# Performance work log

Measured on AMD Instinct MI355X. Metric: run time of the kernel, lower is better.

## Reference

```python
import jax, jax.numpy as jnp
import numpy as np

B, S, DM, H, D = 2, 2048, 1024, 16, 64

def setup_inputs() -> dict:
    key = jax.random.key(0)
    ks = jax.random.split(key, 9)
    def g(k, shape, scale=0.02):
        return jax.random.normal(k, shape, dtype=jnp.float32) * scale
    return {
        "x":  jax.random.normal(ks[0], (B, S, DM), dtype=jnp.float32),
        "Wq": g(ks[1], (DM, H * D)), "bq": g(ks[2], (H * D,)),
        "Wk": g(ks[3], (DM, H * D)), "bk": g(ks[4], (H * D,)),
        "Wv": g(ks[5], (DM, H * D)), "bv": g(ks[6], (H * D,)),
        "Wo": g(ks[7], (H * D, DM)), "bo": g(ks[8], (DM,)),
    }

def reference(x, Wq, bq, Wk, bk, Wv, bv, Wo, bo):
    b, s, _ = x.shape
    # projections -> (B, H, S, D)
    q = (x @ Wq + bq).reshape(b, s, H, D).transpose(0, 2, 1, 3)
    k = (x @ Wk + bk).reshape(b, s, H, D).transpose(0, 2, 1, 3)
    v = (x @ Wv + bv).reshape(b, s, H, D).transpose(0, 2, 1, 3)
    # naive attention: full (B,H,S,S) scores, causal mask, softmax
    scores = jnp.einsum("bhqd,bhkd->bhqk", q, k) / jnp.sqrt(jnp.float32(D))
    causal = jnp.tril(jnp.ones((s, s), dtype=bool))
    scores = jnp.where(causal[None, None], scores, jnp.float32(-jnp.inf))
    weights = jax.nn.softmax(scores, axis=-1)
    out = jnp.einsum("bhqk,bhkd->bhqd", weights, v)  # (B,H,S,D)
    out = out.transpose(0, 2, 1, 3).reshape(b, s, H * D)
    return out @ Wo + bo  # dropout_p = 0 -> identity
```

## Files before the change

### kernel.cpp

```cpp
#include <hip/hip_runtime.h>
#include <hip/hip_bf16.h>

typedef __hip_bfloat16 bf16;
typedef __attribute__((ext_vector_type(8))) short bf16x8;
typedef __attribute__((ext_vector_type(4))) float f32x4;
typedef __attribute__((ext_vector_type(4))) unsigned int u32x4;

#define MFMA_BF16(a, b, c) __builtin_amdgcn_mfma_f32_16x16x32_bf16((a), (b), (c), 0, 0, 0)

static constexpr int B_  = 2;
static constexpr int S_  = 2048;
static constexpr int DM_ = 1024;
static constexpr int H_  = 16;
static constexpr int D_  = 64;
static constexpr int M_  = B_ * S_;

__device__ __forceinline__ void load16(const void* g, void* l) {
  __builtin_amdgcn_global_load_lds(
      (const __attribute__((address_space(1))) void*)g,
      (__attribute__((address_space(3))) void*)l, 16, 0, 0);
}

__device__ __forceinline__ unsigned int pack_bf16(float lo, float hi) {
  const unsigned int ul = __builtin_bit_cast(unsigned short, __float2bfloat16(lo));
  const unsigned int uh = __builtin_bit_cast(unsigned short, __float2bfloat16(hi));
  return (uh << 16) | ul;
}

__global__ void prep_kernel(const float* __restrict__ w0,
                            const float* __restrict__ w1,
                            const float* __restrict__ w2,
                            const float* __restrict__ w3,
                            const float* __restrict__ x,
                            bf16* __restrict__ o0, bf16* __restrict__ o1,
                            bf16* __restrict__ o2, bf16* __restrict__ o3,
                            bf16* __restrict__ xb) {
  if (blockIdx.z == 4) {
    const int blk = blockIdx.y * 32 + blockIdx.x;
#pragma unroll
    for (int rep = 0; rep < 4; ++rep) {
      const int i = blk * 1024 + rep * 256 + threadIdx.x;
      float4 v = ((const float4*)x)[i];
      ushort4 u;
      u.x = __builtin_bit_cast(unsigned short, __float2bfloat16(v.x));
      u.y = __builtin_bit_cast(unsigned short, __float2bfloat16(v.y));
      u.z = __builtin_bit_cast(unsigned short, __float2bfloat16(v.z));
      u.w = __builtin_bit_cast(unsigned short, __float2bfloat16(v.w));
      ((ushort4*)xb)[i] = u;
    }
    return;
  }
  __shared__ float t[32][33];
  const float* in = blockIdx.z == 0 ? w0 : blockIdx.z == 1 ? w1 : blockIdx.z == 2 ? w2 : w3;
  bf16* out = blockIdx.z == 0 ? o0 : blockIdx.z == 1 ? o1 : blockIdx.z == 2 ? o2 : o3;
  int tx = threadIdx.x & 31;
  int ty = threadIdx.x >> 5;
  int r0 = blockIdx.y * 32;
  int c0 = blockIdx.x * 32;
#pragma unroll
  for (int yy = 0; yy < 32; yy += 8)
    t[ty + yy][tx] = in[(size_t)(r0 + ty + yy) * DM_ + c0 + tx];
  __syncthreads();
#pragma unroll
  for (int yy = 0; yy < 32; yy += 8)
    out[(size_t)(c0 + ty + yy) * DM_ + r0 + tx] = __float2bfloat16(t[tx][ty + yy]);
}

__global__ __launch_bounds__(256) void gemm_qkv_kernel(
    const bf16* __restrict__ A, const bf16* __restrict__ Bt,
    const float* __restrict__ bias, const float* __restrict__ bias2,
    const float* __restrict__ bias3, bf16* __restrict__ out, int K) {
  __shared__ bf16 As[2][128 * 32];
  __shared__ bf16 Bs[2][128 * 32];
  const int tid = threadIdx.x;
  const int wid = tid >> 6, lane = tid & 63;
  const int g = lane >> 4, c = lane & 15;
  const int wr = wid >> 1, wc = wid & 1;
  const int bm = blockIdx.x, bn = blockIdx.y;

  f32x4 acc[4][4] = {};

  const char* Ag = (const char*)(A + (size_t)bm * 128 * K);
  const char* Bg = (const char*)(Bt + (size_t)bn * 128 * K);
  const int f0 = tid * 16, f1 = f0 + 4096;
  const int r0 = f0 >> 6, cb0 = f0 & 63;
  const int r1 = f1 >> 6;
  const size_t rowbytes = (size_t)K * 2;

  auto stage = [&](int kt, int bufi) {
    const size_t koff = (size_t)kt * 64;
    load16(Ag + (size_t)r0 * rowbytes + koff + cb0, (char*)As[bufi] + f0);
    load16(Ag + (size_t)r1 * rowbytes + koff + cb0, (char*)As[bufi] + f1);
    load16(Bg + (size_t)r0 * rowbytes + koff + cb0, (char*)Bs[bufi] + f0);
    load16(Bg + (size_t)r1 * rowbytes + koff + cb0, (char*)Bs[bufi] + f1);
  };

  const int NT = K / 32;
  stage(0, 0);
  int cur = 0;
#pragma unroll 1
  for (int kt = 0; kt < NT; ++kt) {
    if (kt + 1 < NT) {
      stage(kt + 1, cur ^ 1);
      asm volatile("s_waitcnt vmcnt(4)" ::: "memory");
    } else {
      asm volatile("s_waitcnt vmcnt(0)" ::: "memory");
    }
    __builtin_amdgcn_s_barrier();

    bf16x8 af[4], bfr[4];
#pragma unroll
    for (int mi = 0; mi < 4; ++mi)
      af[mi] = *(const bf16x8*)&As[cur][(wr * 64 + mi * 16 + c) * 32 + g * 8];
#pragma unroll
    for (int ni = 0; ni < 4; ++ni)
      bfr[ni] = *(const bf16x8*)&Bs[cur][(wc * 64 + ni * 16 + c) * 32 + g * 8];
    __builtin_amdgcn_s_setprio(1);
#pragma unroll
    for (int mi = 0; mi < 4; ++mi)
#pragma unroll
      for (int ni = 0; ni < 4; ++ni)
        acc[mi][ni] = MFMA_BF16(af[mi], bfr[ni], acc[mi][ni]);
    __builtin_amdgcn_s_setprio(0);

    if (kt + 1 < NT) __builtin_amdgcn_s_barrier();
    cur ^= 1;
  }

#pragma unroll
  for (int ni = 0; ni < 4; ++ni) {
    const int n_g = bn * 128 + wc * 64 + ni * 16 + c;
    const int proj = n_g >> 10, ncol = n_g & 1023;
    const float bv = proj == 0 ? bias[ncol] : proj == 1 ? bias2[ncol] : bias3[ncol];
    const int h = ncol >> 6, d = ncol & (D_ - 1);
#pragma unroll
    for (int mi = 0; mi < 4; ++mi) {
#pragma unroll
      for (int r = 0; r < 4; ++r) {
        const int m_g = bm * 128 + wr * 64 + mi * 16 + g * 4 + r;
        const float val = acc[mi][ni][r] + bv;
        const int b = m_g >> 11, s = m_g & (S_ - 1);
        size_t idx = (size_t)proj * 4194304;
        if (proj < 2)
          idx += (((size_t)(b * H_ + h)) * S_ + s) * D_ + d;
        else
          idx += (((size_t)(b * H_ + h)) * D_ + d) * S_ + s;
        out[idx] = __float2bfloat16(val);
      }
    }
  }
}

__global__ __launch_bounds__(256) void gemm_out_kernel(
    const bf16* __restrict__ A, const bf16* __restrict__ Bt,
    const float* __restrict__ bias, float* __restrict__ out, int K) {
  __shared__ bf16 As[2][128 * 32];
  __shared__ bf16 Bs[2][64 * 32];
  const int tid = threadIdx.x;
  const int wid = tid >> 6, lane = tid & 63;
  const int g = lane >> 4, c = lane & 15;
  const int wr = wid >> 1, wc = wid & 1;
  const int bm = blockIdx.x, bn = blockIdx.y;

  f32x4 acc[4][2] = {};

  const char* Ag = (const char*)(A + (size_t)bm * 128 * K);
  const char* Bg = (const char*)(Bt + (size_t)bn * 64 * K);
  const int s0 = tid, s1 = tid + 256;
  const int ra0 = s0 >> 2, ca0 = (s0 & 3) * 16;
  const int ra1 = s1 >> 2, ca1 = (s1 & 3) * 16;
  const int rb = tid >> 2, cb2 = (tid & 3) * 16;
  const size_t rowbytes = (size_t)K * 2;

  auto stage = [&](int kt, int bufi) {
    const size_t koff = (size_t)kt * 64;
    load16(Ag + (size_t)ra0 * rowbytes + koff + ca0, (char*)As[bufi] + s0 * 16);
    load16(Ag + (size_t)ra1 * rowbytes + koff + ca1, (char*)As[bufi] + s1 * 16);
    load16(Bg + (size_t)rb * rowbytes + koff + cb2, (char*)Bs[bufi] + tid * 16);
  };

  const int NT = K / 32;
  stage(0, 0);
  int cur = 0;
#pragma unroll 1
  for (int kt = 0; kt < NT; ++kt) {
    if (kt + 1 < NT) {
      stage(kt + 1, cur ^ 1);
      asm volatile("s_waitcnt vmcnt(3)" ::: "memory");
    } else {
      asm volatile("s_waitcnt vmcnt(0)" ::: "memory");
    }
    __builtin_amdgcn_s_barrier();

    bf16x8 af[4], bfr[2];
#pragma unroll
    for (int mi = 0; mi < 4; ++mi)
      af[mi] = *(const bf16x8*)&As[cur][(wr * 64 + mi * 16 + c) * 32 + g * 8];
#pragma unroll
    for (int ni = 0; ni < 2; ++ni)
      bfr[ni] = *(const bf16x8*)&Bs[cur][(wc * 32 + ni * 16 + c) * 32 + g * 8];
    __builtin_amdgcn_s_setprio(1);
#pragma unroll
    for (int mi = 0; mi < 4; ++mi)
#pragma unroll
      for (int ni = 0; ni < 2; ++ni)
        acc[mi][ni] = MFMA_BF16(af[mi], bfr[ni], acc[mi][ni]);
    __builtin_amdgcn_s_setprio(0);

    if (kt + 1 < NT) __builtin_amdgcn_s_barrier();
    cur ^= 1;
  }

#pragma unroll
  for (int ni = 0; ni < 2; ++ni) {
    const int n_g = bn * 64 + wc * 32 + ni * 16 + c;
    const float bv = bias[n_g];
#pragma unroll
    for (int mi = 0; mi < 4; ++mi) {
#pragma unroll
      for (int r = 0; r < 4; ++r) {
        const int m_g = bm * 128 + wr * 64 + mi * 16 + g * 4 + r;
        out[(size_t)m_g * DM_ + n_g] = acc[mi][ni][r] + bv;
      }
    }
  }
}

__global__ __launch_bounds__(256, 4) void flash_attn_kernel(
    const bf16* __restrict__ Q, const bf16* __restrict__ Kg,
    const bf16* __restrict__ Vt, bf16* __restrict__ Aout) {
  __shared__ bf16 Ks[2][64 * 64];
  __shared__ bf16 Vs[2][64 * 64];
  const int tid = threadIdx.x;
  const int w = tid >> 6, lane = tid & 63;
  const int g = lane >> 4, c = lane & 15;

  const int bid = blockIdx.x;
  const int xcd = bid & 7, loc = bid >> 3;
  const int bh = xcd * 4 + (loc & 3);
  const int u = loc >> 2;
  const int slot = u >> 3, q = u & 7;
  const int j = slot == 0 ? 31 - q : slot == 1 ? 16 + q
              : slot == 2 ? 15 - q : q;
  const int t = j * 4 + w;
  const int b = bh >> 4, h = bh & (H_ - 1);

  const float ALPHA2 = 0.125f * 1.44269504f;
  const float THR2 = 11.5f;
  const float NEG_INF = -__builtin_inff();

  const char* Kbase = (const char*)(Kg + (size_t)bh * S_ * D_);
  const char* Vbase = (const char*)(Vt + (size_t)bh * D_ * S_);
  const int s0 = tid, s1 = tid + 256;
  const int sr0 = s0 >> 3, sq0 = ((s0 & 7) ^ (sr0 & 7)) << 4;
  const int sr1 = s1 >> 3, sq1 = ((s1 & 7) ^ (sr1 & 7)) << 4;

  const bf16* Qp = Q + ((size_t)bh * S_ + t * 16 + c) * D_;
  bf16x8 qf[2];
  qf[0] = *(const bf16x8*)&Qp[g * 8];
  qf[1] = *(const bf16x8*)&Qp[32 + g * 8];

  bf16x8 onesf;
#pragma unroll
  for (int jj = 0; jj < 8; ++jj) onesf[jj] = (short)0x3f80;

  f32x4 o[4] = {};
  f32x4 lacc = {};
  float m = -1000.0f;

  const int rowlim = w * 16 + c;
  const int src0 = ((g & 1) * 2) * 16 + c;
  const int src1 = src0 + 16;
  const bool ghi = (g >= 2);
  const int cs = c & 7;
  int roff[2][4];
#pragma unroll
  for (int kk = 0; kk < 2; ++kk)
#pragma unroll
    for (int n = 0; n < 4; ++n)
      roff[kk][n] = n * 2048 + c * 128 + (((kk * 4 + g) ^ cs) << 4);

  {
    load16(Kbase + sr0 * 128 + sq0, (char*)Ks[0] + s0 * 16);
    load16(Kbase + sr1 * 128 + sq1, (char*)Ks[0] + s1 * 16);
    load16(Vbase + sr0 * 4096 + sq0, (char*)Vs[0] + s0 * 16);
    load16(Vbase + sr1 * 4096 + sq1, (char*)Vs[0] + s1 * 16);
  }
  __syncthreads();

  int cur = 0;
#pragma unroll 1
  for (int kv = 0; kv <= j; ++kv) {
    if (kv < j) {
      const char* Krow = Kbase + (size_t)(kv + 1) * 8192;
      const char* Vcol = Vbase + (size_t)(kv + 1) * 128;
      const int nb = cur ^ 1;
      load16(Krow + sr0 * 128 + sq0, (char*)Ks[nb] + s0 * 16);
      load16(Krow + sr1 * 128 + sq1, (char*)Ks[nb] + s1 * 16);
      load16(Vcol + sr0 * 4096 + sq0, (char*)Vs[nb] + s0 * 16);
      load16(Vcol + sr1 * 4096 + sq1, (char*)Vs[nb] + s1 * 16);
    }

    const char* Kt = (const char*)Ks[cur];
    const char* Vtile = (const char*)Vs[cur];
    bf16x8 kf[2][4];
#pragma unroll
    for (int kk = 0; kk < 2; ++kk)
#pragma unroll
      for (int n = 0; n < 4; ++n)
        kf[kk][n] = *(const bf16x8*)(Kt + roff[kk][n]);

    f32x4 st[4] = {};
    __builtin_amdgcn_s_setprio(1);
#pragma unroll
    for (int n = 0; n < 4; ++n) {
      st[n] = MFMA_BF16(kf[0][n], qf[0], st[n]);
      st[n] = MFMA_BF16(kf[1][n], qf[1], st[n]);
    }
    __builtin_amdgcn_s_setprio(0);

    bf16x8 vf[2][4];
#pragma unroll
    for (int kk = 0; kk < 2; ++kk)
#pragma unroll
      for (int n = 0; n < 4; ++n)
        vf[kk][n] = *(const bf16x8*)(Vtile + roff[kk][n]);

    float aa[4][4];
#pragma unroll
    for (int n = 0; n < 4; ++n)
#pragma unroll
      for (int r = 0; r < 4; ++r)
        aa[n][r] = fmaf(st[n][r], ALPHA2, -m);
    if (kv == j) {
#pragma unroll
      for (int n = 0; n < 4; ++n)
#pragma unroll
        for (int r = 0; r < 4; ++r)
          if (n * 16 + g * 4 + r > rowlim) aa[n][r] = NEG_INF;
    }

    float lm;
    {
      float t0 = fmaxf(fmaxf(aa[0][0], aa[0][1]), fmaxf(aa[0][2], aa[0][3]));
      float t1 = fmaxf(fmaxf(aa[1][0], aa[1][1]), fmaxf(aa[1][2], aa[1][3]));
      float t2 = fmaxf(fmaxf(aa[2][0], aa[2][1]), fmaxf(aa[2][2], aa[2][3]));
      float t3 = fmaxf(fmaxf(aa[3][0], aa[3][1]), fmaxf(aa[3][2], aa[3][3]));
      lm = fmaxf(fmaxf(t0, t1), fmaxf(t2, t3));
    }

    if (__any(lm > THR2)) {
      float dm = fmaxf(lm, __shfl_xor(lm, 16, 64));
      dm = fmaxf(dm, __shfl_xor(dm, 32, 64));
      const float sh = fmaxf(dm, 0.0f);
      const float sc = __builtin_amdgcn_exp2f(-sh);
      m += sh;
#pragma unroll
      for (int r = 0; r < 4; ++r) lacc[r] *= sc;
#pragma unroll
      for (int n = 0; n < 4; ++n)
#pragma unroll
        for (int r = 0; r < 4; ++r) o[n][r] *= sc;
#pragma unroll
      for (int n = 0; n < 4; ++n)
#pragma unroll
        for (int r = 0; r < 4; ++r) aa[n][r] -= sh;
    }

    float p[4][4];
#pragma unroll
    for (int n = 0; n < 4; ++n)
#pragma unroll
      for (int r = 0; r < 4; ++r) p[n][r] = __builtin_amdgcn_exp2f(aa[n][r]);

    unsigned int dw[4][2];
#pragma unroll
    for (int n = 0; n < 4; ++n) {
      dw[n][0] = pack_bf16(p[n][0], p[n][1]);
      dw[n][1] = pack_bf16(p[n][2], p[n][3]);
    }

#pragma unroll
    for (int kk = 0; kk < 2; ++kk) {
      unsigned int bb[4];
      {
        unsigned int lo = __shfl(dw[kk * 2][0], src0, 64);
        unsigned int hi = __shfl(dw[kk * 2 + 1][0], src0, 64);
        bb[0] = ghi ? hi : lo;
      }
      {
        unsigned int lo = __shfl(dw[kk * 2][1], src0, 64);
        unsigned int hi = __shfl(dw[kk * 2 + 1][1], src0, 64);
        bb[1] = ghi ? hi : lo;
      }
      {
        unsigned int lo = __shfl(dw[kk * 2][0], src1, 64);
        unsigned int hi = __shfl(dw[kk * 2 + 1][0], src1, 64);
        bb[2] = ghi ? hi : lo;
      }
      {
        unsigned int lo = __shfl(dw[kk * 2][1], src1, 64);
        unsigned int hi = __shfl(dw[kk * 2 + 1][1], src1, 64);
        bb[3] = ghi ? hi : lo;
      }
      u32x4 bbv = {bb[0], bb[1], bb[2], bb[3]};
      bf16x8 pb = __builtin_bit_cast(bf16x8, bbv);
      __builtin_amdgcn_s_setprio(1);
#pragma unroll
      for (int n = 0; n < 4; ++n) o[n] = MFMA_BF16(vf[kk][n], pb, o[n]);
      lacc = MFMA_BF16(onesf, pb, lacc);
      __builtin_amdgcn_s_setprio(0);
    }

    __syncthreads();
    cur ^= 1;
  }

  const float inv = 1.0f / lacc[0];

  bf16* Arow = Aout + ((size_t)b * S_ + t * 16 + c) * (H_ * D_) + h * D_;
#pragma unroll
  for (int n = 0; n < 4; ++n) {
    ushort4 u2;
    u2.x = __builtin_bit_cast(unsigned short, __float2bfloat16(o[n][0] * inv));
    u2.y = __builtin_bit_cast(unsigned short, __float2bfloat16(o[n][1] * inv));
    u2.z = __builtin_bit_cast(unsigned short, __float2bfloat16(o[n][2] * inv));
    u2.w = __builtin_bit_cast(unsigned short, __float2bfloat16(o[n][3] * inv));
    *(ushort4*)&Arow[n * 16 + g * 4] = u2;
  }
}


extern "C" void kernel_launch(void* const* d_in, const int* in_sizes, int n_in,
                              void* d_out, int out_size, void* d_ws, size_t ws_size,
                              hipStream_t stream) {
  (void)in_sizes; (void)n_in; (void)out_size; (void)ws_size;
  const float* x  = (const float*)d_in[0];
  const float* Wq = (const float*)d_in[1];
  const float* bq = (const float*)d_in[2];
  const float* Wk = (const float*)d_in[3];
  const float* bk = (const float*)d_in[4];
  const float* Wv = (const float*)d_in[5];
  const float* bv = (const float*)d_in[6];
  const float* Wo = (const float*)d_in[7];
  const float* bo = (const float*)d_in[8];
  float* out = (float*)d_out;

  char* ws = (char*)d_ws;
  bf16* xb  = (bf16*)(ws);
  bf16* Wqt = (bf16*)(ws + (8u << 20));
  bf16* Wkt = (bf16*)(ws + (10u << 20));
  bf16* Wvt = (bf16*)(ws + (12u << 20));
  bf16* Wot = (bf16*)(ws + (14u << 20));
  bf16* Qb  = (bf16*)(ws + (16u << 20));
  bf16* Kb  = (bf16*)(ws + (24u << 20));
  bf16* Vtb = (bf16*)(ws + (32u << 20));
  bf16* Ab  = xb;

  prep_kernel<<<dim3(32, 32, 5), 256, 0, stream>>>(
      Wq, Wk, Wv, Wo, x, Wqt, Wkt, Wvt, Wot, xb);

  gemm_qkv_kernel<<<dim3(32, 24), 256, 0, stream>>>(
      xb, Wqt, bq, bk, bv, Qb, DM_);

  flash_attn_kernel<<<dim3(1024), 256, 0, stream>>>(Qb, Kb, Vtb, Ab);

  gemm_out_kernel<<<dim3(32, 16), 256, 0, stream>>>(Ab, Wot, bo, out, DM_);
}
```

Measured before the change: 113.2 us.

## Process two 16-row query tiles per wave to double K/V reuse

Each wave now owns two consecutive 16-row query tiles, so a block covers 128 query rows and each K/V tile loaded into LDS serves twice as many queries. The grid is halved from 1024 to 512 blocks and the diagonal masking is reworked for the wider block, with the longest blocks scheduled first. The aim is to cut LDS fill and global K/V traffic per unit of work. In exchange it doubles the accumulator and score registers, which may lower occupancy under launch_bounds(256,4), and fewer blocks with uneven causal lengths may hurt load balance.

```diff
diff --git a/kernel.cpp b/kernel.cpp
--- a/kernel.cpp
+++ b/kernel.cpp
@@ -238,11 +238,10 @@
   const int bid = blockIdx.x;
   const int xcd = bid & 7, loc = bid >> 3;
   const int bh = xcd * 4 + (loc & 3);
-  const int u = loc >> 2;
-  const int slot = u >> 3, q = u & 7;
-  const int j = slot == 0 ? 31 - q : slot == 1 ? 16 + q
-              : slot == 2 ? 15 - q : q;
-  const int t = j * 4 + w;
+  const int v = 15 - (loc >> 2);
+  const int base = v * 8 + w * 2;
+  const int dtile = base >> 2;
+  const int jtop = 2 * v + 1;
   const int b = bh >> 4, h = bh & (H_ - 1);
 
   const float ALPHA2 = 0.125f * 1.44269504f;
@@ -255,20 +254,23 @@
   const int sr0 = s0 >> 3, sq0 = ((s0 & 7) ^ (sr0 & 7)) << 4;
   const int sr1 = s1 >> 3, sq1 = ((s1 & 7) ^ (sr1 & 7)) << 4;
 
-  const bf16* Qp = Q + ((size_t)bh * S_ + t * 16 + c) * D_;
-  bf16x8 qf[2];
-  qf[0] = *(const bf16x8*)&Qp[g * 8];
-  qf[1] = *(const bf16x8*)&Qp[32 + g * 8];
+  const bf16* QpA = Q + ((size_t)bh * S_ + base * 16 + c) * D_;
+  bf16x8 qfA0 = *(const bf16x8*)&QpA[g * 8];
+  bf16x8 qfA1 = *(const bf16x8*)&QpA[32 + g * 8];
+  const bf16* QpB = QpA + 16 * D_;
+  bf16x8 qfB0 = *(const bf16x8*)&QpB[g * 8];
+  bf16x8 qfB1 = *(const bf16x8*)&QpB[32 + g * 8];
 
   bf16x8 onesf;
 #pragma unroll
   for (int jj = 0; jj < 8; ++jj) onesf[jj] = (short)0x3f80;
 
-  f32x4 o[4] = {};
-  f32x4 lacc = {};
-  float m = -1000.0f;
-
-  const int rowlim = w * 16 + c;
+  f32x4 oA[4] = {}, oB[4] = {};
+  f32x4 laccA = {}, laccB = {};
+  float mA = -1000.0f, mB = -1000.0f;
+
+  const int rowlimA = (base & 3) * 16 + c;
+  const int rowlimB = rowlimA + 16;
   const int src0 = ((g & 1) * 2) * 16 + c;
   const int src1 = src0 + 16;
   const bool ghi = (g >= 2);
@@ -290,8 +292,8 @@
 
   int cur = 0;
 #pragma unroll 1
-  for (int kv = 0; kv <= j; ++kv) {
-    if (kv < j) {
+  for (int kv = 0; kv <= jtop; ++kv) {
+    if (kv < jtop) {
       const char* Krow = Kbase + (size_t)(kv + 1) * 8192;
       const char* Vcol = Vbase + (size_t)(kv + 1) * 128;
       const int nb = cur ^ 1;
@@ -310,12 +312,14 @@
       for (int n = 0; n < 4; ++n)
         kf[kk][n] = *(const bf16x8*)(Kt + roff[kk][n]);
 
-    f32x4 st[4] = {};
+    f32x4 stA[4] = {}, stB[4] = {};
     __builtin_amdgcn_s_setprio(1);
 #pragma unroll
     for (int n = 0; n < 4; ++n) {
-      st[n] = MFMA_BF16(kf[0][n], qf[0], st[n]);
-      st[n] = MFMA_BF16(kf[1][n], qf[1], st[n]);
+      stA[n] = MFMA_BF16(kf[0][n], qfA0, stA[n]);
+      stA[n] = MFMA_BF16(kf[1][n], qfA1, stA[n]);
+      stB[n] = MFMA_BF16(kf[0][n], qfB0, stB[n]);
+      stB[n] = MFMA_BF16(kf[1][n], qfB1, stB[n]);
     }
     __builtin_amdgcn_s_setprio(0);
 
@@ -326,89 +330,171 @@
       for (int n = 0; n < 4; ++n)
         vf[kk][n] = *(const bf16x8*)(Vtile + roff[kk][n]);
 
-    float aa[4][4];
-#pragma unroll
-    for (int n = 0; n < 4; ++n)
-#pragma unroll
-      for (int r = 0; r < 4; ++r)
-        aa[n][r] = fmaf(st[n][r], ALPHA2, -m);
-    if (kv == j) {
+    const bool onDiag = (kv >= dtile);
+
+    float pA[4][4];
+    {
+      float aa[4][4];
 #pragma unroll
       for (int n = 0; n < 4; ++n)
 #pragma unroll
         for (int r = 0; r < 4; ++r)
-          if (n * 16 + g * 4 + r > rowlim) aa[n][r] = NEG_INF;
-    }
-
-    float lm;
+          aa[n][r] = fmaf(stA[n][r], ALPHA2, -mA);
+      if (onDiag) {
+        const int lim = (kv == dtile) ? rowlimA : -1;
+#pragma unroll
+        for (int n = 0; n < 4; ++n)
+#pragma unroll
+          for (int r = 0; r < 4; ++r)
+            if (n * 16 + g * 4 + r > lim) aa[n][r] = NEG_INF;
+      }
+      float lm;
+      {
+        float t0 = fmaxf(fmaxf(aa[0][0], aa[0][1]), fmaxf(aa[0][2], aa[0][3]));
+        float t1 = fmaxf(fmaxf(aa[1][0], aa[1][1]), fmaxf(aa[1][2], aa[1][3]));
+        float t2 = fmaxf(fmaxf(aa[2][0], aa[2][1]), fmaxf(aa[2][2], aa[2][3]));
+        float t3 = fmaxf(fmaxf(aa[3][0], aa[3][1]), fmaxf(aa[3][2], aa[3][3]));
+        lm = fmaxf(fmaxf(t0, t1), fmaxf(t2, t3));
+      }
+      if (__any(lm > THR2)) {
+        float dm = fmaxf(lm, __shfl_xor(lm, 16, 64));
+        dm = fmaxf(dm, __shfl_xor(dm, 32, 64));
+        const float sh = fmaxf(dm, 0.0f);
+        const float sc = __builtin_amdgcn_exp2f(-sh);
+        mA += sh;
+#pragma unroll
+        for (int r = 0; r < 4; ++r) laccA[r] *= sc;
+#pragma unroll
+        for (int n = 0; n < 4; ++n)
+#pragma unroll
+          for (int r = 0; r < 4; ++r) oA[n][r] *= sc;
+#pragma unroll
+        for (int n = 0; n < 4; ++n)
+#pragma unroll
+          for (int r = 0; r < 4; ++r) aa[n][r] -= sh;
+      }
+#pragma unroll
+      for (int n = 0; n < 4; ++n)
+#pragma unroll
+        for (int r = 0; r < 4; ++r) pA[n][r] = __builtin_amdgcn_exp2f(aa[n][r]);
+    }
+
+    float pB[4][4];
     {
-      float t0 = fmaxf(fmaxf(aa[0][0], aa[0][1]), fmaxf(aa[0][2], aa[0][3]));
-      float t1 = fmaxf(fmaxf(aa[1][0], aa[1][1]), fmaxf(aa[1][2], aa[1][3]));
-      float t2 = fmaxf(fmaxf(aa[2][0], aa[2][1]), fmaxf(aa[2][2], aa[2][3]));
-      float t3 = fmaxf(fmaxf(aa[3][0], aa[3][1]), fmaxf(aa[3][2], aa[3][3]));
-      lm = fmaxf(fmaxf(t0, t1), fmaxf(t2, t3));
-    }
-
-    if (__any(lm > THR2)) {
-      float dm = fmaxf(lm, __shfl_xor(lm, 16, 64));
-      dm = fmaxf(dm, __shfl_xor(dm, 32, 64));
-      const float sh = fmaxf(dm, 0.0f);
-      const float sc = __builtin_amdgcn_exp2f(-sh);
-      m += sh;
-#pragma unroll
-      for (int r = 0; r < 4; ++r) lacc[r] *= sc;
+      float aa[4][4];
 #pragma unroll
       for (int n = 0; n < 4; ++n)
 #pragma unroll
-        for (int r = 0; r < 4; ++r) o[n][r] *= sc;
+        for (int r = 0; r < 4; ++r)
+          aa[n][r] = fmaf(stB[n][r], ALPHA2, -mB);
+      if (onDiag) {
+        const int lim = (kv == dtile) ? rowlimB : -1;
+#pragma unroll
+        for (int n = 0; n < 4; ++n)
+#pragma unroll
+          for (int r = 0; r < 4; ++r)
+            if (n * 16 + g * 4 + r > lim) aa[n][r] = NEG_INF;
+      }
+      float lm;
+      {
+        float t0 = fmaxf(fmaxf(aa[0][0], aa[0][1]), fmaxf(aa[0][2], aa[0][3]));
+        float t1 = fmaxf(fmaxf(aa[1][0], aa[1][1]), fmaxf(aa[1][2], aa[1][3]));
+        float t2 = fmaxf(fmaxf(aa[2][0], aa[2][1]), fmaxf(aa[2][2], aa[2][3]));
+        float t3 = fmaxf(fmaxf(aa[3][0], aa[3][1]), fmaxf(aa[3][2], aa[3][3]));
+        lm = fmaxf(fmaxf(t0, t1), fmaxf(t2, t3));
+      }
+      if (__any(lm > THR2)) {
+        float dm = fmaxf(lm, __shfl_xor(lm, 16, 64));
+        dm = fmaxf(dm, __shfl_xor(dm, 32, 64));
+        const float sh = fmaxf(dm, 0.0f);
+        const float sc = __builtin_amdgcn_exp2f(-sh);
+        mB += sh;
+#pragma unroll
+        for (int r = 0; r < 4; ++r) laccB[r] *= sc;
+#pragma unroll
+        for (int n = 0; n < 4; ++n)
+#pragma unroll
+          for (int r = 0; r < 4; ++r) oB[n][r] *= sc;
+#pragma unroll
+        for (int n = 0; n < 4; ++n)
+#pragma unroll
+          for (int r = 0; r < 4; ++r) aa[n][r] -= sh;
+      }
 #pragma unroll
       for (int n = 0; n < 4; ++n)
 #pragma unroll
-        for (int r = 0; r < 4; ++r) aa[n][r] -= sh;
-    }
-
-    float p[4][4];
-#pragma unroll
-    for (int n = 0; n < 4; ++n)
-#pragma unroll
-      for (int r = 0; r < 4; ++r) p[n][r] = __builtin_amdgcn_exp2f(aa[n][r]);
-
-    unsigned int dw[4][2];
+        for (int r = 0; r < 4; ++r) pB[n][r] = __builtin_amdgcn_exp2f(aa[n][r]);
+    }
+
+    unsigned int dwA[4][2], dwB[4][2];
 #pragma unroll
     for (int n = 0; n < 4; ++n) {
-      dw[n][0] = pack_bf16(p[n][0], p[n][1]);
-      dw[n][1] = pack_bf16(p[n][2], p[n][3]);
+      dwA[n][0] = pack_bf16(pA[n][0], pA[n][1]);
+      dwA[n][1] = pack_bf16(pA[n][2], pA[n][3]);
+      dwB[n][0] = pack_bf16(pB[n][0], pB[n][1]);
+      dwB[n][1] = pack_bf16(pB[n][2], pB[n][3]);
     }
 
 #pragma unroll
     for (int kk = 0; kk < 2; ++kk) {
       unsigned int bb[4];
       {
-        unsigned int lo = __shfl(dw[kk * 2][0], src0, 64);
-        unsigned int hi = __shfl(dw[kk * 2 + 1][0], src0, 64);
+        unsigned int lo = __shfl(dwA[kk * 2][0], src0, 64);
+        unsigned int hi = __shfl(dwA[kk * 2 + 1][0], src0, 64);
         bb[0] = ghi ? hi : lo;
       }
       {
-        unsigned int lo = __shfl(dw[kk * 2][1], src0, 64);
-        unsigned int hi = __shfl(dw[kk * 2 + 1][1], src0, 64);
+        unsigned int lo = __shfl(dwA[kk * 2][1], src0, 64);
+        unsigned int hi = __shfl(dwA[kk * 2 + 1][1], src0, 64);
         bb[1] = ghi ? hi : lo;
       }
       {
-        unsigned int lo = __shfl(dw[kk * 2][0], src1, 64);
-        unsigned int hi = __shfl(dw[kk * 2 + 1][0], src1, 64);
+        unsigned int lo = __shfl(dwA[kk * 2][0], src1, 64);
+        unsigned int hi = __shfl(dwA[kk * 2 + 1][0], src1, 64);
         bb[2] = ghi ? hi : lo;
       }
       {
-        unsigned int lo = __shfl(dw[kk * 2][1], src1, 64);
-        unsigned int hi = __shfl(dw[kk * 2 + 1][1], src1, 64);
+        unsigned int lo = __shfl(dwA[kk * 2][1], src1, 64);
+        unsigned int hi = __shfl(dwA[kk * 2 + 1][1], src1, 64);
         bb[3] = ghi ? hi : lo;
       }
       u32x4 bbv = {bb[0], bb[1], bb[2], bb[3]};
       bf16x8 pb = __builtin_bit_cast(bf16x8, bbv);
       __builtin_amdgcn_s_setprio(1);
 #pragma unroll
-      for (int n = 0; n < 4; ++n) o[n] = MFMA_BF16(vf[kk][n], pb, o[n]);
-      lacc = MFMA_BF16(onesf, pb, lacc);
+      for (int n = 0; n < 4; ++n) oA[n] = MFMA_BF16(vf[kk][n], pb, oA[n]);
+      laccA = MFMA_BF16(onesf, pb, laccA);
+      __builtin_amdgcn_s_setprio(0);
+    }
+#pragma unroll
+    for (int kk = 0; kk < 2; ++kk) {
+      unsigned int bb[4];
+      {
+        unsigned int lo = __shfl(dwB[kk * 2][0], src0, 64);
+        unsigned int hi = __shfl(dwB[kk * 2 + 1][0], src0, 64);
+        bb[0] = ghi ? hi : lo;
+      }
+      {
+        unsigned int lo = __shfl(dwB[kk * 2][1], src0, 64);
+        unsigned int hi = __shfl(dwB[kk * 2 + 1][1], src0, 64);
+        bb[1] = ghi ? hi : lo;
+      }
+      {
+        unsigned int lo = __shfl(dwB[kk * 2][0], src1, 64);
+        unsigned int hi = __shfl(dwB[kk * 2 + 1][0], src1, 64);
+        bb[2] = ghi ? hi : lo;
+      }
+      {
+        unsigned int lo = __shfl(dwB[kk * 2][1], src1, 64);
+        unsigned int hi = __shfl(dwB[kk * 2 + 1][1], src1, 64);
+        bb[3] = ghi ? hi : lo;
+      }
+      u32x4 bbv = {bb[0], bb[1], bb[2], bb[3]};
+      bf16x8 pb = __builtin_bit_cast(bf16x8, bbv);
+      __builtin_amdgcn_s_setprio(1);
+#pragma unroll
+      for (int n = 0; n < 4; ++n) oB[n] = MFMA_BF16(vf[kk][n], pb, oB[n]);
+      laccB = MFMA_BF16(onesf, pb, laccB);
       __builtin_amdgcn_s_setprio(0);
     }
 
@@ -416,17 +502,27 @@
     cur ^= 1;
   }
 
-  const float inv = 1.0f / lacc[0];
-
-  bf16* Arow = Aout + ((size_t)b * S_ + t * 16 + c) * (H_ * D_) + h * D_;
+  const float invA = 1.0f / laccA[0];
+  bf16* ArowA = Aout + ((size_t)b * S_ + base * 16 + c) * (H_ * D_) + h * D_;
 #pragma unroll
   for (int n = 0; n < 4; ++n) {
     ushort4 u2;
-    u2.x = __builtin_bit_cast(unsigned short, __float2bfloat16(o[n][0] * inv));
-    u2.y = __builtin_bit_cast(unsigned short, __float2bfloat16(o[n][1] * inv));
-    u2.z = __builtin_bit_cast(unsigned short, __float2bfloat16(o[n][2] * inv));
-    u2.w = __builtin_bit_cast(unsigned short, __float2bfloat16(o[n][3] * inv));
-    *(ushort4*)&Arow[n * 16 + g * 4] = u2;
+    u2.x = __builtin_bit_cast(unsigned short, __float2bfloat16(oA[n][0] * invA));
+    u2.y = __builtin_bit_cast(unsigned short, __float2bfloat16(oA[n][1] * invA));
+    u2.z = __builtin_bit_cast(unsigned short, __float2bfloat16(oA[n][2] * invA));
+    u2.w = __builtin_bit_cast(unsigned short, __float2bfloat16(oA[n][3] * invA));
+    *(ushort4*)&ArowA[n * 16 + g * 4] = u2;
+  }
+  const float invB = 1.0f / laccB[0];
+  bf16* ArowB = ArowA + (size_t)16 * (H_ * D_);
+#pragma unroll
+  for (int n = 0; n < 4; ++n) {
+    ushort4 u2;
+    u2.x = __builtin_bit_cast(unsigned short, __float2bfloat16(oB[n][0] * invB));
+    u2.y = __builtin_bit_cast(unsigned short, __float2bfloat16(oB[n][1] * invB));
+    u2.z = __builtin_bit_cast(unsigned short, __float2bfloat16(oB[n][2] * invB));
+    u2.w = __builtin_bit_cast(unsigned short, __float2bfloat16(oB[n][3] * invB));
+    *(ushort4*)&ArowB[n * 16 + g * 4] = u2;
   }
 }
 
@@ -463,7 +559,7 @@
   gemm_qkv_kernel<<<dim3(32, 24), 256, 0, stream>>>(
       xb, Wqt, bq, bk, bv, Qb, DM_);
 
-  flash_attn_kernel<<<dim3(1024), 256, 0, stream>>>(Qb, Kb, Vtb, Ab);
+  flash_attn_kernel<<<dim3(512), 256, 0, stream>>>(Qb, Kb, Vtb, Ab);
 
   gemm_out_kernel<<<dim3(32, 16), 256, 0, stream>>>(Ab, Wot, bo, out, DM_);
 }
```

New measurement: 167.4 us. 1.48x slower.
